# Performance work log

Hardware: AMD Instinct MI355X
Metric: run time of the kernel (lower is better)

Reference implementation:

```python
import jax, jax.numpy as jnp
import numpy as np

N = 50000
HID = 128
NH = 4
E_RES, E_SEQ, E_KNN = 100000, 100000, 200000
BN_EPS = 1e-5
NEG_SLOPE = 0.2


def _gat(h, src, dst, W, al, ar, resW, b):
    """DGL-style GATConv (eval mode: feat_drop off, residual=True, bias).
    h: (N, in), W/resW: (in, H*out), al/ar: (H, out), b: (H*out,)"""
    Hh, out = al.shape
    feat = (h @ W).reshape(N, Hh, out)                 # (N, H, out)
    el = jnp.sum(feat * al, axis=-1)                   # (N, H)
    er = jnp.sum(feat * ar, axis=-1)                   # (N, H)
    e = jax.nn.leaky_relu(el[src] + er[dst], NEG_SLOPE)  # (E, H)
    # edge softmax over incoming edges of each dst node (numerically stable)
    m = jax.ops.segment_max(e, dst, num_segments=N)    # (N, H)
    ex = jnp.exp(e - m[dst])
    s = jax.ops.segment_sum(ex, dst, num_segments=N)
    a = ex / s[dst]                                    # (E, H)
    msg = a[:, :, None] * feat[src]                    # (E, H, out)
    rst = jax.ops.segment_sum(msg, dst, num_segments=N)  # (N, H, out)
    return rst + (h @ resW).reshape(N, Hh, out) + b.reshape(1, Hh, out)


def _hetero(h, src_res, dst_res, src_seq, dst_seq, src_knn, dst_knn, W, al, ar, resW, b):
    # HeteroGraphConv with aggregate='sum' over relations, then mean over heads
    r = _gat(h, src_res, dst_res, W[0], al[0], ar[0], resW[0], b[0])
    r = r + _gat(h, src_seq, dst_seq, W[1], al[1], ar[1], resW[1], b[1])
    r = r + _gat(h, src_knn, dst_knn, W[2], al[2], ar[2], resW[2], b[2])
    return jnp.mean(r, axis=1)                         # (N, out)


def setup_inputs() -> dict:
    key = jax.random.key(0)
    ks = iter(jax.random.split(key, 32))
    inp = {}
    inp["x"] = jax.random.normal(next(ks), (N, HID), jnp.float32)
    inp["src_res"] = jax.random.randint(next(ks), (E_RES,), 0, N, jnp.int32)
    inp["dst_res"] = jax.random.randint(next(ks), (E_RES,), 0, N, jnp.int32)
    inp["src_seq"] = jax.random.randint(next(ks), (E_SEQ,), 0, N, jnp.int32)
    inp["dst_seq"] = jax.random.randint(next(ks), (E_SEQ,), 0, N, jnp.int32)
    inp["src_knn"] = jax.random.randint(next(ks), (E_KNN,), 0, N, jnp.int32)
    inp["dst_knn"] = jax.random.randint(next(ks), (E_KNN,), 0, N, jnp.int32)
    sc = 0.05
    for l in (0, 1):
        inp[f"W{l}"] = jax.random.normal(next(ks), (3, HID, NH * HID), jnp.float32) * sc
        inp[f"al{l}"] = jax.random.normal(next(ks), (3, NH, HID), jnp.float32) * sc
        inp[f"ar{l}"] = jax.random.normal(next(ks), (3, NH, HID), jnp.float32) * sc
        inp[f"resW{l}"] = jax.random.normal(next(ks), (3, HID, NH * HID), jnp.float32) * sc
        inp[f"b{l}"] = jax.random.normal(next(ks), (3, NH * HID), jnp.float32) * sc
    inp["fc_W"] = jax.random.normal(next(ks), (HID, HID), jnp.float32) * sc
    inp["fc_b"] = jax.random.normal(next(ks), (HID,), jnp.float32) * sc
    inp["bn_gamma"] = jnp.ones((HID,), jnp.float32)
    inp["bn_beta"] = jnp.zeros((HID,), jnp.float32)
    inp["bn_mean"] = jax.random.normal(next(ks), (HID,), jnp.float32) * sc
    inp["bn_var"] = jax.random.uniform(next(ks), (HID,), jnp.float32)
    return inp


def reference(x, src_res, dst_res, src_seq, dst_seq, src_knn, dst_knn,
              W0, al0, ar0, resW0, b0, W1, al1, ar1, resW1, b1,
              fc_W, fc_b, bn_gamma, bn_beta, bn_mean, bn_var):
    # layer 0: hetero GAT, head-mean, fc + ReLU + BatchNorm (eval), dropout=identity
    h = _hetero(x, src_res, dst_res, src_seq, dst_seq, src_knn, dst_knn,
                W0, al0, ar0, resW0, b0)
    h = jax.nn.relu(h @ fc_W + fc_b)
    h = (h - bn_mean) / jnp.sqrt(bn_var + BN_EPS) * bn_gamma + bn_beta
    # layer 1 (final): hetero GAT, head-mean
    out = _hetero(h, src_res, dst_res, src_seq, dst_seq, src_knn, dst_knn,
                  W1, al1, ar1, resW1, b1)
    return out
```

## Files before the change

### kernel.cpp

```cpp
#include <hip/hip_runtime.h>
#include <hip/hip_bf16.h>
#include <math.h>
#include <stdint.h>

#define NNODES 50000
#define SCHUNK 4096
#define AW 1664
#define XOFF 1536

typedef __bf16 bf16x8 __attribute__((ext_vector_type(8)));
typedef float f32x4 __attribute__((ext_vector_type(4)));
typedef unsigned short u16;
typedef unsigned int u32;

__device__ __forceinline__ float lrelu(float x){ return x >= 0.f ? x : 0.2f*x; }
__device__ __forceinline__ float b2f(u16 u){ union{ u32 i; float f; } c; c.i = ((u32)u)<<16; return c.f; }
__device__ __forceinline__ float lo2f(u32 v){ union{ u32 i; float f; } c; c.i = v<<16; return c.f; }
__device__ __forceinline__ float hi2f(u32 v){ union{ u32 i; float f; } c; c.i = v & 0xffff0000u; return c.f; }
__device__ __forceinline__ u16 f2b(float f){ __hip_bfloat16 h = __float2bfloat16(f); return *(u16*)&h; }
__device__ __forceinline__ u32 packbf(float a, float b){ return (u32)f2b(a) | ((u32)f2b(b) << 16); }

__global__ void prep_b(const float* __restrict__ W0, const float* __restrict__ W1,
                       const float* __restrict__ resW0, const float* __restrict__ resW1,
                       const float* __restrict__ b0, const float* __restrict__ b1,
                       u16* __restrict__ Btb, float* __restrict__ biasf)
{
    int gid = blockIdx.x*blockDim.x + threadIdx.x;
    if (gid < 2*128*AW){
        int l = gid / (128*AW);
        int rem = gid - l*(128*AW);
        int c = rem / AW;
        int j = rem - c*AW;
        const float* W  = l ? W1 : W0;
        const float* rw = l ? resW1 : resW0;
        float v;
        if (j < XOFF){
            int r = j >> 9, h = (j >> 7) & 3, k = j & 127;
            v = 0.25f * W[(size_t)r*65536 + (size_t)k*512 + h*128 + c];
        } else {
            int k = j - XOFF;
            float s = 0.f;
            for (int r = 0; r < 3; ++r)
                for (int h = 0; h < 4; ++h)
                    s += rw[(size_t)r*65536 + (size_t)k*512 + h*128 + c];
            v = 0.25f * s;
        }
        Btb[gid] = f2b(v);
    }
    if (gid < 256){
        int l = gid >> 7, c = gid & 127;
        const float* bb = l ? b1 : b0;
        float s = 0.f;
        for (int r = 0; r < 3; ++r)
            for (int h = 0; h < 4; ++h)
                s += bb[r*512 + h*128 + c];
        biasf[gid] = 0.25f*s;
    }
}

__global__ void prep_wl(const float* __restrict__ W0, const float* __restrict__ W1,
                        const float* __restrict__ al0, const float* __restrict__ ar0,
                        const float* __restrict__ al1, const float* __restrict__ ar1,
                        const float* __restrict__ fcW,
                        u16* __restrict__ wlb, u16* __restrict__ fcWtb)
{
    int gid = blockIdx.x*blockDim.x + threadIdx.x;
    if (gid < 2*128*128){
        int l = gid >> 14;
        int col = (gid >> 7) & 127;
        int k = gid & 127;
        float v = 0.f;
        if (col < 24){
            int r = col >> 3, lr = (col >> 2) & 1, h = col & 3;
            const float* W = l ? W1 : W0;
            const float* av = l ? (lr ? ar1 : al1) : (lr ? ar0 : al0);
            const float* wrow = W + (size_t)r*65536 + (size_t)k*512 + h*128;
            const float* arow = av + r*512 + h*128;
            for (int cc = 0; cc < 128; ++cc) v += wrow[cc]*arow[cc];
        }
        wlb[gid] = f2b(v);
    }
    if (gid < 128*128){
        int k = gid & 127, n = gid >> 7;
        fcWtb[gid] = f2b(fcW[k*128 + n]);
    }
}

__global__ __launch_bounds__(256) void xprep_kernel(const float* __restrict__ x,
    u16* __restrict__ Ax, const u16* __restrict__ wl, float* __restrict__ el, int M)
{
    __shared__ u16 Xs[64*136];
    __shared__ u16 Ws[32*136];
    const int tid = threadIdx.x;
    const int row0 = blockIdx.x*64;
    #pragma unroll
    for (int p = 0; p < 2; ++p){
        int idx = tid + p*256;
        int c = idx >> 4, kc = (idx & 15)*8;
        float4 v = make_float4(0.f,0.f,0.f,0.f);
        if (c < 24) v = *(const float4*)(wl + c*128 + kc);
        *(float4*)&Ws[c*136 + kc] = v;
    }
    int r = tid >> 2, cq = (tid & 3)*32;
    int grow = row0 + r;
    if (grow < M){
        #pragma unroll
        for (int i = 0; i < 8; ++i){
            float4 v = *(const float4*)(x + (size_t)grow*128 + cq + i*4);
            ushort4 o;
            o.x = f2b(v.x); o.y = f2b(v.y); o.z = f2b(v.z); o.w = f2b(v.w);
            *(ushort4*)(Ax + (size_t)grow*AW + cq + i*4) = o;
            *(ushort4*)&Xs[r*136 + cq + i*4] = o;
        }
    } else {
        ushort4 z; z.x=0; z.y=0; z.z=0; z.w=0;
        #pragma unroll
        for (int i = 0; i < 8; ++i) *(ushort4*)&Xs[r*136 + cq + i*4] = z;
    }
    __syncthreads();
    const int lane = tid & 63, wave = tid >> 6;
    const int r16 = lane & 15, quad = lane >> 4;
    f32x4 acc0 = {}, acc1 = {};
    #pragma unroll
    for (int ks = 0; ks < 4; ++ks){
        int ko = ks*32 + quad*8;
        bf16x8 a  = *(const bf16x8*)&Xs[(wave*16 + r16)*136 + ko];
        bf16x8 b0 = *(const bf16x8*)&Ws[r16*136 + ko];
        bf16x8 b1 = *(const bf16x8*)&Ws[(16 + r16)*136 + ko];
        acc0 = __builtin_amdgcn_mfma_f32_16x16x32_bf16(a, b0, acc0, 0,0,0);
        acc1 = __builtin_amdgcn_mfma_f32_16x16x32_bf16(a, b1, acc1, 0,0,0);
    }
    #pragma unroll
    for (int p = 0; p < 4; ++p){
        int row = row0 + wave*16 + quad*4 + p;
        if (row < M){
            el[(size_t)row*32 + r16] = acc0[p];
            if (r16 < 8) el[(size_t)row*32 + 16 + r16] = acc1[p];
        }
    }
}

__global__ void hist_all(const int* __restrict__ d0, const int* __restrict__ d1,
                         const int* __restrict__ d2, int e0, int e1, int e2,
                         int* __restrict__ cnt)
{
    int g = blockIdx.x*blockDim.x + threadIdx.x;
    if (g >= e0 + e1 + e2) return;
    int rel, idx;
    if (g < e0){ rel = 0; idx = g; }
    else if (g < e0 + e1){ rel = 1; idx = g - e0; }
    else { rel = 2; idx = g - e0 - e1; }
    const int* d = rel == 0 ? d0 : (rel == 1 ? d1 : d2);
    atomicAdd(cnt + (size_t)rel*NNODES + d[idx], 1);
}

__global__ __launch_bounds__(256) void scan_part(const int* __restrict__ cnt_all,
                                                 int* __restrict__ partials, int Nn, int nblk)
{
    int rel = blockIdx.y, blk = blockIdx.x;
    const int* cnt = cnt_all + (size_t)rel*Nn;
    int tid = threadIdx.x;
    int i0 = blk*SCHUNK + tid*16;
    int s = 0;
    #pragma unroll
    for (int k = 0; k < 4; ++k){
        int idx = i0 + k*4;
        if (idx + 3 < Nn){ int4 v = *(const int4*)(cnt + idx); s += v.x+v.y+v.z+v.w; }
        else { for (int j = 0; j < 4; ++j) if (idx+j < Nn) s += cnt[idx+j]; }
    }
    #pragma unroll
    for (int off = 1; off < 64; off <<= 1) s += __shfl_xor(s, off);
    __shared__ int ws[4];
    if ((tid & 63) == 0) ws[tid>>6] = s;
    __syncthreads();
    if (tid == 0) partials[rel*nblk + blk] = ws[0]+ws[1]+ws[2]+ws[3];
}

__global__ __launch_bounds__(256) void scan_write(const int* __restrict__ cnt_all,
                                                  const int* __restrict__ partials,
                                                  int* __restrict__ rp_all, int* __restrict__ cur_all,
                                                  int Nn, int nblk)
{
    int rel = blockIdx.y, blk = blockIdx.x;
    const int* cnt = cnt_all + (size_t)rel*Nn;
    int* rp  = rp_all  + (size_t)rel*(Nn+1);
    int* cur = cur_all + (size_t)rel*Nn;
    int tid = threadIdx.x;
    __shared__ int sOff;
    __shared__ int wsum[4];
    if (tid == 0){
        int o = 0;
        for (int b = 0; b < blk; ++b) o += partials[rel*nblk + b];
        sOff = o;
        if (blk == 0){
            int t = 0;
            for (int b = 0; b < nblk; ++b) t += partials[rel*nblk + b];
            rp[Nn] = t;
        }
    }
    int i0 = blk*SCHUNK + tid*16;
    int v[16];
    int s = 0;
    #pragma unroll
    for (int k = 0; k < 16; ++k){
        int idx = i0 + k;
        v[k] = (idx < Nn) ? cnt[idx] : 0;
        s += v[k];
    }
    int lane = tid & 63;
    int incl = s;
    #pragma unroll
    for (int off = 1; off < 64; off <<= 1){
        int t = __shfl_up(incl, off);
        if (lane >= off) incl += t;
    }
    if (lane == 63) wsum[tid>>6] = incl;
    __syncthreads();
    int woff = 0;
    for (int w = 0; w < (tid>>6); ++w) woff += wsum[w];
    int ex = sOff + woff + incl - s;
    #pragma unroll
    for (int k = 0; k < 16; ++k){
        int idx = i0 + k;
        if (idx < Nn){ rp[idx] = ex; cur[idx] = ex; }
        ex += v[k];
    }
}

__global__ void scatter_all(const int* __restrict__ s0, const int* __restrict__ s1,
                            const int* __restrict__ s2,
                            const int* __restrict__ d0, const int* __restrict__ d1,
                            const int* __restrict__ d2, int e0, int e1, int e2,
                            int* __restrict__ cur, int* __restrict__ colb,
                            int* __restrict__ dste)
{
    int g = blockIdx.x*blockDim.x + threadIdx.x;
    if (g >= e0 + e1 + e2) return;
    int rel, idx, coff;
    if (g < e0){ rel = 0; idx = g; coff = 0; }
    else if (g < e0 + e1){ rel = 1; idx = g - e0; coff = e0; }
    else { rel = 2; idx = g - e0 - e1; coff = e0 + e1; }
    const int* sp = rel == 0 ? s0 : (rel == 1 ? s1 : s2);
    const int* dp = rel == 0 ? d0 : (rel == 1 ? d1 : d2);
    int d = dp[idx];
    int pos = atomicAdd(cur + (size_t)rel*NNODES + d, 1);
    colb[coff + pos] = sp[idx];
    dste[coff + pos] = d;
}

__global__ void wprep(const int* __restrict__ colb, const int* __restrict__ dste,
                      int e0, int e01, int etot,
                      const float* __restrict__ el_all, ushort4* __restrict__ colw)
{
    int j = blockIdx.x*blockDim.x + threadIdx.x;
    if (j >= etot) return;
    int rel = (j < e0) ? 0 : ((j < e01) ? 1 : 2);
    int src = colb[j], dst = dste[j];
    float4 es = *(const float4*)(el_all + (size_t)src*32 + rel*8);
    float4 ed = *(const float4*)(el_all + (size_t)dst*32 + rel*8 + 4);
    ushort4 o;
    o.x = f2b(__expf(lrelu(es.x + ed.x)));
    o.y = f2b(__expf(lrelu(es.y + ed.y)));
    o.z = f2b(__expf(lrelu(es.z + ed.z)));
    o.w = f2b(__expf(lrelu(es.w + ed.w)));
    colw[j] = o;
}

__global__ __launch_bounds__(256) void agg2(const int* __restrict__ rowp_all,
    const int* __restrict__ colb_all, const ushort4* __restrict__ colw_all,
    int e0, int e01,
    const u16* __restrict__ Ax, u16* __restrict__ Abuf, int Nn)
{
    const int rel = blockIdx.y;
    const int tid = threadIdx.x;
    const int lane = tid & 63;
    const int hl = lane & 31;
    const int halfbase = lane & 32;
    const int n = (blockIdx.x*256 + tid) >> 5;
    if (n >= Nn) return;
    const int* rowp = rowp_all + (size_t)rel*(Nn+1);
    const int coff = (rel == 0) ? 0 : ((rel == 1) ? e0 : e01);
    const int* colb = colb_all + coff;
    const ushort4* colw = colw_all + coff;
    u16* op = Abuf + (size_t)n*AW + rel*512 + hl*4;

    int beg = rowp[n], end = rowp[n+1];
    if (beg >= end){
        uint2 z; z.x = 0; z.y = 0;
        #pragma unroll
        for (int h = 0; h < 4; ++h) *(uint2*)(op + h*128) = z;
        return;
    }
    float acc[4][4] = {};
    float us0 = 0.f, us1 = 0.f, us2 = 0.f, us3 = 0.f;
    for (int eb = beg; eb < end; eb += 32){
        int j = eb + hl;
        int s = 0; uint2 w2; w2.x = 0; w2.y = 0;
        if (j < end){
            s = colb[j];
            w2 = *(const uint2*)&colw[j];
        }
        us0 += lo2f(w2.x); us1 += hi2f(w2.x);
        us2 += lo2f(w2.y); us3 += hi2f(w2.y);
        int cnt = min(32, end - eb);
        for (int t = 0; t < cnt; ++t){
            int lsrc = halfbase + t;
            int st = __shfl(s, lsrc);
            u32 wa = (u32)__shfl((int)w2.x, lsrc);
            u32 wb = (u32)__shfl((int)w2.y, lsrc);
            float w0 = lo2f(wa), w1 = hi2f(wa), w2f = lo2f(wb), w3 = hi2f(wb);
            uint2 xv = *(const uint2*)(Ax + (size_t)st*AW + hl*4);
            float x0 = lo2f(xv.x), x1 = hi2f(xv.x), x2 = lo2f(xv.y), x3 = hi2f(xv.y);
            acc[0][0] = fmaf(w0, x0, acc[0][0]); acc[0][1] = fmaf(w0, x1, acc[0][1]);
            acc[0][2] = fmaf(w0, x2, acc[0][2]); acc[0][3] = fmaf(w0, x3, acc[0][3]);
            acc[1][0] = fmaf(w1, x0, acc[1][0]); acc[1][1] = fmaf(w1, x1, acc[1][1]);
            acc[1][2] = fmaf(w1, x2, acc[1][2]); acc[1][3] = fmaf(w1, x3, acc[1][3]);
            acc[2][0] = fmaf(w2f, x0, acc[2][0]); acc[2][1] = fmaf(w2f, x1, acc[2][1]);
            acc[2][2] = fmaf(w2f, x2, acc[2][2]); acc[2][3] = fmaf(w2f, x3, acc[2][3]);
            acc[3][0] = fmaf(w3, x0, acc[3][0]); acc[3][1] = fmaf(w3, x1, acc[3][1]);
            acc[3][2] = fmaf(w3, x2, acc[3][2]); acc[3][3] = fmaf(w3, x3, acc[3][3]);
        }
    }
    #pragma unroll
    for (int off = 1; off < 32; off <<= 1){
        us0 += __shfl_xor(us0, off); us1 += __shfl_xor(us1, off);
        us2 += __shfl_xor(us2, off); us3 += __shfl_xor(us3, off);
    }
    float inv[4] = {1.f/us0, 1.f/us1, 1.f/us2, 1.f/us3};
    #pragma unroll
    for (int h = 0; h < 4; ++h){
        uint2 o;
        o.x = packbf(acc[h][0]*inv[h], acc[h][1]*inv[h]);
        o.y = packbf(acc[h][2]*inv[h], acc[h][3]*inv[h]);
        *(uint2*)(op + h*128) = o;
    }
}

template<int EPI, int ELR>
__global__ __launch_bounds__(256) void gemm_f(
    const u16* __restrict__ A, int Astride, int K,
    const u16* __restrict__ Bt,
    float* __restrict__ Cf, u16* __restrict__ Cb, int Cstride, int M,
    const float* __restrict__ bias, const float* __restrict__ gamma,
    const float* __restrict__ beta, const float* __restrict__ mean,
    const float* __restrict__ var,
    const u16* __restrict__ wl, float* __restrict__ el)
{
    __shared__ u16 smem[13056];
    u16* As = smem;
    u16* Bs = smem + 4096;
    const int tid = threadIdx.x;
    const int row0 = blockIdx.x*64;
    const int lane = tid & 63, wave = tid >> 6;
    const int wm = (wave >> 1)*32, wn = (wave & 1)*64;
    const int r16 = lane & 15, quad = lane >> 4;
    const int swzbase = r16 & 7;
    f32x4 acc[2][4] = {};

    for (int k0 = 0; k0 < K; k0 += 64){
        #pragma unroll
        for (int p = 0; p < 2; ++p){
            int idx = tid + p*256;
            int r = idx >> 3, kc = idx & 7;
            int gr = row0 + r;
            float4 v = make_float4(0.f,0.f,0.f,0.f);
            if (gr < M) v = *(const float4*)(A + (size_t)gr*Astride + k0 + kc*8);
            *(float4*)&As[r*64 + ((kc ^ (r & 7)) << 3)] = v;
        }
        #pragma unroll
        for (int p = 0; p < 4; ++p){
            int idx = tid + p*256;
            int r = idx >> 3, kc = idx & 7;
            float4 v = *(const float4*)(Bt + (size_t)r*K + k0 + kc*8);
            *(float4*)&Bs[r*64 + ((kc ^ (r & 7)) << 3)] = v;
        }
        __syncthreads();
        #pragma unroll
        for (int ks = 0; ks < 2; ++ks){
            int swz = ((ks*4 + quad) ^ swzbase) << 3;
            bf16x8 a0 = *(const bf16x8*)&As[(wm + r16)*64 + swz];
            bf16x8 a1 = *(const bf16x8*)&As[(wm + 16 + r16)*64 + swz];
            #pragma unroll
            for (int j = 0; j < 4; ++j){
                bf16x8 b = *(const bf16x8*)&Bs[(wn + j*16 + r16)*64 + swz];
                acc[0][j] = __builtin_amdgcn_mfma_f32_16x16x32_bf16(a0, b, acc[0][j], 0,0,0);
                acc[1][j] = __builtin_amdgcn_mfma_f32_16x16x32_bf16(a1, b, acc[1][j], 0,0,0);
            }
        }
        __syncthreads();
    }

    u16* Cs = smem;
    u16* Ws = smem + 64*136;
    if (ELR){
        #pragma unroll
        for (int p = 0; p < 2; ++p){
            int idx = tid + p*256;
            int c = idx >> 4, kc = (idx & 15)*8;
            float4 v = make_float4(0.f,0.f,0.f,0.f);
            if (c < 24) v = *(const float4*)(wl + c*128 + kc);
            *(float4*)&Ws[c*136 + kc] = v;
        }
    }
    #pragma unroll
    for (int i = 0; i < 2; ++i){
        #pragma unroll
        for (int p = 0; p < 4; ++p){
            int rl = wm + i*16 + quad*4 + p;
            int row = row0 + rl;
            #pragma unroll
            for (int j = 0; j < 4; ++j){
                int col = wn + j*16 + r16;
                float v = acc[i][j][p] + bias[col];
                if (EPI == 2){
                    float t = fmaxf(v, 0.f);
                    v = (t - mean[col]) * rsqrtf(var[col] + 1e-5f) * gamma[col] + beta[col];
                }
                u16 vb = f2b(v);
                if (row < M){
                    if (EPI == 1) Cf[(size_t)row*Cstride + col] = v;
                    else          Cb[(size_t)row*Cstride + col] = vb;
                }
                if (ELR) Cs[rl*136 + col] = vb;
            }
        }
    }
    if (ELR){
        __syncthreads();
        f32x4 e0 = {}, e1 = {};
        #pragma unroll
        for (int ks = 0; ks < 4; ++ks){
            int ko = ks*32 + quad*8;
            bf16x8 a  = *(const bf16x8*)&Cs[(wave*16 + r16)*136 + ko];
            bf16x8 b0 = *(const bf16x8*)&Ws[r16*136 + ko];
            bf16x8 b1 = *(const bf16x8*)&Ws[(16 + r16)*136 + ko];
            e0 = __builtin_amdgcn_mfma_f32_16x16x32_bf16(a, b0, e0, 0,0,0);
            e1 = __builtin_amdgcn_mfma_f32_16x16x32_bf16(a, b1, e1, 0,0,0);
        }
        #pragma unroll
        for (int p = 0; p < 4; ++p){
            int row = row0 + wave*16 + quad*4 + p;
            if (row < M){
                el[(size_t)row*32 + r16] = e0[p];
                if (r16 < 8) el[(size_t)row*32 + 16 + r16] = e1[p];
            }
        }
    }
}

static inline char* align256(char* p){ return (char*)(((uintptr_t)p + 255) & ~(uintptr_t)255); }

extern "C" void kernel_launch(void* const* d_in, const int* in_sizes, int n_in,
                              void* d_out, int out_size, void* d_ws, size_t ws_size,
                              hipStream_t stream)
{
    const float* x      = (const float*)d_in[0];
    const int* srcs[3]  = {(const int*)d_in[1], (const int*)d_in[3], (const int*)d_in[5]};
    const int* dsts[3]  = {(const int*)d_in[2], (const int*)d_in[4], (const int*)d_in[6]};
    const int  E[3]     = {in_sizes[1], in_sizes[3], in_sizes[5]};
    const float* W0     = (const float*)d_in[7];
    const float* al0    = (const float*)d_in[8];
    const float* ar0    = (const float*)d_in[9];
    const float* resW0  = (const float*)d_in[10];
    const float* b0     = (const float*)d_in[11];
    const float* W1     = (const float*)d_in[12];
    const float* al1    = (const float*)d_in[13];
    const float* ar1    = (const float*)d_in[14];
    const float* resW1  = (const float*)d_in[15];
    const float* b1     = (const float*)d_in[16];
    const float* fcW    = (const float*)d_in[17];
    const float* fcb    = (const float*)d_in[18];
    const float* gamma  = (const float*)d_in[19];
    const float* beta   = (const float*)d_in[20];
    const float* bmean  = (const float*)d_in[21];
    const float* bvar   = (const float*)d_in[22];
    float* out = (float*)d_out;

    char* p = (char*)d_ws;
    u16*   Abuf  = (u16*)p;   p += (size_t)NNODES*AW*2;    p = align256(p);
    float* el    = (float*)p; p += (size_t)NNODES*32*4;    p = align256(p);
    u16*   hmb   = (u16*)p;   p += (size_t)NNODES*128*2;   p = align256(p);
    int*   cnt   = (int*)p;   p += (size_t)3*NNODES*4;     p = align256(p);
    int*   rowp  = (int*)p;   p += (size_t)3*(NNODES+1)*4; p = align256(p);
    int*   cur   = (int*)p;   p += (size_t)3*NNODES*4;     p = align256(p);
    int*   colb  = (int*)p;   p += (size_t)(E[0]+E[1]+E[2])*4; p = align256(p);
    int*   dste  = (int*)p;   p += (size_t)(E[0]+E[1]+E[2])*4; p = align256(p);
    ushort4* colw= (ushort4*)p; p += (size_t)(E[0]+E[1]+E[2])*8; p = align256(p);
    u16*   Btb   = (u16*)p;   p += (size_t)2*128*AW*2;     p = align256(p);
    u16*   wlb   = (u16*)p;   p += (size_t)2*128*128*2;    p = align256(p);
    u16*   fcWtb = (u16*)p;   p += (size_t)128*128*2;      p = align256(p);
    float* biasf = (float*)p; p += (size_t)2*128*4;        p = align256(p);
    int*   parts = (int*)p;   p += (size_t)3*64*4;

    const int NBLK = (NNODES + SCHUNK - 1)/SCHUNK;
    const int MB = (NNODES + 63)/64;
    const int AGGBLKS = (NNODES + 7)/8;
    const int ETOT = E[0] + E[1] + E[2];
    dim3 blk(256);
    u16* Ax = Abuf + XOFF;

    hipMemsetAsync(cnt, 0, (size_t)3*NNODES*sizeof(int), stream);
    prep_b <<<(2*128*AW + 255)/256, blk, 0, stream>>>(W0, W1, resW0, resW1, b0, b1, Btb, biasf);
    prep_wl<<<(2*128*128 + 255)/256, blk, 0, stream>>>(W0, W1, al0, ar0, al1, ar1, fcW, wlb, fcWtb);
    xprep_kernel<<<MB, blk, 0, stream>>>(x, Ax, wlb, el, NNODES);
    hist_all<<<(ETOT + 255)/256, blk, 0, stream>>>(dsts[0], dsts[1], dsts[2], E[0], E[1], E[2], cnt);
    scan_part <<<dim3(NBLK,3), blk, 0, stream>>>(cnt, parts, NNODES, NBLK);
    scan_write<<<dim3(NBLK,3), blk, 0, stream>>>(cnt, parts, rowp, cur, NNODES, NBLK);
    scatter_all<<<(ETOT + 255)/256, blk, 0, stream>>>(srcs[0], srcs[1], srcs[2],
                                                      dsts[0], dsts[1], dsts[2],
                                                      E[0], E[1], E[2], cur, colb, dste);

    wprep<<<(ETOT + 255)/256, blk, 0, stream>>>(colb, dste, E[0], E[0]+E[1], ETOT, el, colw);
    agg2<<<dim3(AGGBLKS,3), blk, 0, stream>>>(rowp, colb, colw, E[0], E[0]+E[1], Ax, Abuf, NNODES);
    gemm_f<4,0><<<MB, blk, 0, stream>>>(Abuf, AW, AW, Btb, nullptr, hmb, 128, NNODES,
                                        biasf, nullptr, nullptr, nullptr, nullptr, nullptr, nullptr);
    gemm_f<2,1><<<MB, blk, 0, stream>>>(hmb, 128, 128, fcWtb, nullptr, Ax, AW, NNODES,
                                        fcb, gamma, beta, bmean, bvar, wlb + 16384, el);

    wprep<<<(ETOT + 255)/256, blk, 0, stream>>>(colb, dste, E[0], E[0]+E[1], ETOT, el, colw);
    agg2<<<dim3(AGGBLKS,3), blk, 0, stream>>>(rowp, colb, colw, E[0], E[0]+E[1], Ax, Abuf, NNODES);
    gemm_f<1,0><<<MB, blk, 0, stream>>>(Abuf, AW, AW, Btb + (size_t)128*AW, out, nullptr, 128, NNODES,
                                        biasf + 128, nullptr, nullptr, nullptr, nullptr, nullptr, nullptr);
}
```

Measured before the change: 391.8 us.

## Double-buffer GEMM shared memory tiles with register prefetch of next K slice

The GEMM main loop now prefetches the next K slice of A and B into registers while MFMAs run on the current tile, and alternates between two shared-memory buffers so one barrier per iteration is enough. Global load latency is meant to overlap with compute. In exchange, shared memory per block nearly doubles (48KB), which may reduce occupancy, and more registers are needed for the prefetched data.

Result: slower. 567.1 us (+44.8%).

```diff
diff --git a/kernel.cpp b/kernel.cpp
--- a/kernel.cpp
+++ b/kernel.cpp
@@ -346,9 +346,7 @@
     const float* __restrict__ var,
     const u16* __restrict__ wl, float* __restrict__ el)
 {
-    __shared__ u16 smem[13056];
-    u16* As = smem;
-    u16* Bs = smem + 4096;
+    __shared__ u16 smem[24576];
     const int tid = threadIdx.x;
     const int row0 = blockIdx.x*64;
     const int lane = tid & 63, wave = tid >> 6;
@@ -357,24 +355,51 @@
     const int swzbase = r16 & 7;
     f32x4 acc[2][4] = {};
 
-    for (int k0 = 0; k0 < K; k0 += 64){
-        #pragma unroll
-        for (int p = 0; p < 2; ++p){
-            int idx = tid + p*256;
-            int r = idx >> 3, kc = idx & 7;
-            int gr = row0 + r;
-            float4 v = make_float4(0.f,0.f,0.f,0.f);
-            if (gr < M) v = *(const float4*)(A + (size_t)gr*Astride + k0 + kc*8);
-            *(float4*)&As[r*64 + ((kc ^ (r & 7)) << 3)] = v;
-        }
-        #pragma unroll
-        for (int p = 0; p < 4; ++p){
-            int idx = tid + p*256;
-            int r = idx >> 3, kc = idx & 7;
-            float4 v = *(const float4*)(Bt + (size_t)r*K + k0 + kc*8);
-            *(float4*)&Bs[r*64 + ((kc ^ (r & 7)) << 3)] = v;
-        }
+    int aOff[2]; const u16* aG[2]; bool aOk[2];
+    #pragma unroll
+    for (int p = 0; p < 2; ++p){
+        int idx = tid + p*256;
+        int r = idx >> 3, kc = idx & 7;
+        aOff[p] = r*64 + ((kc ^ (r & 7)) << 3);
+        int gr = row0 + r;
+        aOk[p] = gr < M;
+        aG[p] = A + (size_t)(aOk[p] ? gr : 0)*Astride + kc*8;
+    }
+    int bOff[4]; const u16* bG[4];
+    #pragma unroll
+    for (int p = 0; p < 4; ++p){
+        int idx = tid + p*256;
+        int r = idx >> 3, kc = idx & 7;
+        bOff[p] = r*64 + ((kc ^ (r & 7)) << 3);
+        bG[p] = Bt + (size_t)r*K + kc*8;
+    }
+
+    const int NIT = K >> 6;
+    float4 ra[2], rb[4];
+    #pragma unroll
+    for (int p = 0; p < 2; ++p)
+        ra[p] = aOk[p] ? *(const float4*)(aG[p]) : make_float4(0.f,0.f,0.f,0.f);
+    #pragma unroll
+    for (int p = 0; p < 4; ++p)
+        rb[p] = *(const float4*)(bG[p]);
+
+    for (int it = 0; it < NIT; ++it){
+        u16* As = smem + (it & 1)*12288;
+        u16* Bs = As + 4096;
+        #pragma unroll
+        for (int p = 0; p < 2; ++p) *(float4*)&As[aOff[p]] = ra[p];
+        #pragma unroll
+        for (int p = 0; p < 4; ++p) *(float4*)&Bs[bOff[p]] = rb[p];
         __syncthreads();
+        if (it + 1 < NIT){
+            int k0 = (it + 1) << 6;
+            #pragma unroll
+            for (int p = 0; p < 2; ++p)
+                ra[p] = aOk[p] ? *(const float4*)(aG[p] + k0) : make_float4(0.f,0.f,0.f,0.f);
+            #pragma unroll
+            for (int p = 0; p < 4; ++p)
+                rb[p] = *(const float4*)(bG[p] + k0);
+        }
         #pragma unroll
         for (int ks = 0; ks < 2; ++ks){
             int swz = ((ks*4 + quad) ^ swzbase) << 3;
@@ -387,12 +412,12 @@
                 acc[1][j] = __builtin_amdgcn_mfma_f32_16x16x32_bf16(a1, b, acc[1][j], 0,0,0);
             }
         }
-        __syncthreads();
     }
 
     u16* Cs = smem;
     u16* Ws = smem + 64*136;
     if (ELR){
+        __syncthreads();
         #pragma unroll
         for (int p = 0; p < 2; ++p){
             int idx = tid + p*256;
```
